# Performance work log

Hardware: AMD Instinct MI355X
Metric: run time of the kernel (lower is better)

## Reference

```python
import jax, jax.numpy as jnp
import numpy as np

G = 500          # num graphs
NODES_PER_G = 1000
EDGES_PER_G = 2000
N = G * NODES_PER_G   # 500_000 total nodes
E = G * EDGES_PER_G   # 1_000_000 total edges
DN, DE, DG, DO = 128, 64, 128, 128


def setup_inputs() -> dict:
    key = jax.random.key(0)
    ks = jax.random.split(key, 7)
    return {
        "node_features": jax.random.normal(ks[0], (N, DN), dtype=jnp.float32),
        "edge_features": jax.random.normal(ks[1], (E, DE), dtype=jnp.float32),
        "global_features": jax.random.normal(ks[2], (G, DG), dtype=jnp.float32),
        "W_node": jax.random.normal(ks[3], (DO, DN), dtype=jnp.float32) / np.sqrt(DN),
        "W_edges": jax.random.normal(ks[4], (DO, DE), dtype=jnp.float32) / np.sqrt(DE),
        "W_global": jax.random.normal(ks[5], (DO, DG), dtype=jnp.float32) / np.sqrt(DG),
        "bias": jax.random.normal(ks[6], (DO,), dtype=jnp.float32) * 0.01,
        "num_nodes_by_graph": jnp.full((G,), NODES_PER_G, dtype=jnp.int32),
        "num_edges_by_graph": jnp.full((G,), EDGES_PER_G, dtype=jnp.int32),
    }


def _segment_mean(feats, lengths, num_segments, total):
    # segment ids from per-graph lengths (segment_lengths_to_ids)
    ids = jnp.repeat(jnp.arange(num_segments, dtype=jnp.int32), lengths,
                     total_repeat_length=total)
    s = jax.ops.segment_sum(feats, ids, num_segments=num_segments)
    cnt = jnp.maximum(lengths, 1).astype(feats.dtype)[:, None]
    return s / cnt


def reference(node_features, edge_features, global_features,
              W_node, W_edges, W_global, bias,
              num_nodes_by_graph, num_edges_by_graph):
    # mean-aggregate nodes/edges per graph, then linear projections summed
    node_agg = _segment_mean(node_features, num_nodes_by_graph, G, N)   # [G, DN]
    edge_agg = _segment_mean(edge_features, num_edges_by_graph, G, E)   # [G, DE]
    out = (jnp.einsum('gd,od->go', node_agg, W_node)
           + jnp.einsum('gd,od->go', edge_agg, W_edges)
           + jnp.einsum('gd,od->go', global_features, W_global)
           + bias)
    return out
```

## Files before the change

kernel.cpp:

```cpp
#include <hip/hip_runtime.h>


#define DN 128
#define DE 64
#define DO 128
#define NODE_SPLIT 4
#define EDGE_SPLIT 8

__global__ __launch_bounds__(512) void scan_offsets_kernel(
    const int* __restrict__ nlen, const int* __restrict__ elen, int G,
    int* __restrict__ noff, int* __restrict__ eoff)
{
    __shared__ int sn[512], se[512];
    __shared__ int carry_n, carry_e;
    const int t = threadIdx.x;
    if (t == 0) { carry_n = 0; carry_e = 0; }
    __syncthreads();

    for (int base = 0; base < G; base += 512) {
        const int idx = base + t;
        const int vn = (idx < G) ? nlen[idx] : 0;
        const int ve = (idx < G) ? elen[idx] : 0;
        sn[t] = vn; se[t] = ve;
        __syncthreads();
        for (int off = 1; off < 512; off <<= 1) {
            const int an = (t >= off) ? sn[t - off] : 0;
            const int ae = (t >= off) ? se[t - off] : 0;
            __syncthreads();
            sn[t] += an; se[t] += ae;
            __syncthreads();
        }
        if (idx < G) {
            noff[idx] = carry_n + sn[t] - vn;
            eoff[idx] = carry_e + se[t] - ve;
        }
        __syncthreads();
        if (t == 0) {
            const int last = (G - base < 512) ? (G - base - 1) : 511;
            carry_n += sn[last];
            carry_e += se[last];
        }
        __syncthreads();
    }
}

__global__ __launch_bounds__(256) void agg_kernel(
    const float* __restrict__ nodes, const float* __restrict__ edges,
    const int* __restrict__ noff, const int* __restrict__ eoff,
    const int* __restrict__ nlen, const int* __restrict__ elen,
    float* __restrict__ nsum, float* __restrict__ esum, int G)
{
    __shared__ float4 sm[256];
    const int b = blockIdx.x;
    const int t = threadIdx.x;

    if (b < G * NODE_SPLIT) {
        const int g = b / NODE_SPLIT;
        const int c = b % NODE_SPLIT;
        const int len = nlen[g];
        const int off = noff[g];
        const int chunk = (len + NODE_SPLIT - 1) / NODE_SPLIT;
        const int r0 = c * chunk;
        const int r1 = (r0 + chunk < len) ? (r0 + chunk) : len;

        const int col = t & 31;
        const int rl  = t >> 5;
        float4 acc = make_float4(0.f, 0.f, 0.f, 0.f);
        const float4* __restrict__ base = (const float4*)nodes;
        for (int r = r0 + rl; r < r1; r += 8) {
            const float4 v = base[(size_t)(off + r) * (DN / 4) + col];
            acc.x += v.x; acc.y += v.y; acc.z += v.z; acc.w += v.w;
        }
        sm[t] = acc;
        __syncthreads();
        for (int s = 128; s >= 32; s >>= 1) {
            if (t < s) {
                const float4 o = sm[t + s];
                sm[t].x += o.x; sm[t].y += o.y; sm[t].z += o.z; sm[t].w += o.w;
            }
            __syncthreads();
        }
        if (t < 32) {
            const float4 v = sm[t];
            float* dst = &nsum[(size_t)g * DN + col * 4];
            atomicAdd(dst + 0, v.x);
            atomicAdd(dst + 1, v.y);
            atomicAdd(dst + 2, v.z);
            atomicAdd(dst + 3, v.w);
        }
    } else {
        const int bb = b - G * NODE_SPLIT;
        const int g = bb / EDGE_SPLIT;
        const int c = bb % EDGE_SPLIT;
        const int len = elen[g];
        const int off = eoff[g];
        const int chunk = (len + EDGE_SPLIT - 1) / EDGE_SPLIT;
        const int r0 = c * chunk;
        const int r1 = (r0 + chunk < len) ? (r0 + chunk) : len;

        const int col = t & 15;
        const int rl  = t >> 4;
        float4 acc = make_float4(0.f, 0.f, 0.f, 0.f);
        const float4* __restrict__ base = (const float4*)edges;
        for (int r = r0 + rl; r < r1; r += 16) {
            const float4 v = base[(size_t)(off + r) * (DE / 4) + col];
            acc.x += v.x; acc.y += v.y; acc.z += v.z; acc.w += v.w;
        }
        sm[t] = acc;
        __syncthreads();
        for (int s = 128; s >= 16; s >>= 1) {
            if (t < s) {
                const float4 o = sm[t + s];
                sm[t].x += o.x; sm[t].y += o.y; sm[t].z += o.z; sm[t].w += o.w;
            }
            __syncthreads();
        }
        if (t < 16) {
            const float4 v = sm[t];
            float* dst = &esum[(size_t)g * DE + col * 4];
            atomicAdd(dst + 0, v.x);
            atomicAdd(dst + 1, v.y);
            atomicAdd(dst + 2, v.z);
            atomicAdd(dst + 3, v.w);
        }
    }
}

__global__ __launch_bounds__(128) void finalize_kernel(
    const float* __restrict__ nsum, const float* __restrict__ esum,
    const float* __restrict__ glob,
    const float* __restrict__ Wn, const float* __restrict__ We,
    const float* __restrict__ Wg, const float* __restrict__ bias,
    const int* __restrict__ nlen, const int* __restrict__ elen,
    float* __restrict__ out)
{
    __shared__ float sn[DN], se_[DE], sg[DN];
    const int g = blockIdx.x;
    const int o = threadIdx.x;

    const int nl = nlen[g];
    const int el = elen[g];
    const float inv_n = 1.0f / (float)((nl > 1) ? nl : 1);
    const float inv_e = 1.0f / (float)((el > 1) ? el : 1);

    sn[o] = nsum[(size_t)g * DN + o] * inv_n;
    sg[o] = glob[(size_t)g * DN + o];
    if (o < DE) se_[o] = esum[(size_t)g * DE + o] * inv_e;
    __syncthreads();

    float acc = bias[o];
    const float4* __restrict__ wn = (const float4*)(Wn + (size_t)o * DN);
    const float4* __restrict__ wg = (const float4*)(Wg + (size_t)o * DN);
    const float4* __restrict__ we = (const float4*)(We + (size_t)o * DE);
    const float4* s4n = (const float4*)sn;
    const float4* s4g = (const float4*)sg;
    const float4* s4e = (const float4*)se_;

    #pragma unroll
    for (int i = 0; i < DN / 4; ++i) {
        const float4 a = wn[i], v = s4n[i];
        acc += a.x * v.x + a.y * v.y + a.z * v.z + a.w * v.w;
    }
    #pragma unroll
    for (int i = 0; i < DN / 4; ++i) {
        const float4 a = wg[i], v = s4g[i];
        acc += a.x * v.x + a.y * v.y + a.z * v.z + a.w * v.w;
    }
    #pragma unroll
    for (int i = 0; i < DE / 4; ++i) {
        const float4 a = we[i], v = s4e[i];
        acc += a.x * v.x + a.y * v.y + a.z * v.z + a.w * v.w;
    }
    out[(size_t)g * DO + o] = acc;
}

extern "C" void kernel_launch(void* const* d_in, const int* in_sizes, int n_in,
                              void* d_out, int out_size, void* d_ws, size_t ws_size,
                              hipStream_t stream)
{
    const float* nodes = (const float*)d_in[0];
    const float* edges = (const float*)d_in[1];
    const float* glob  = (const float*)d_in[2];
    const float* Wn    = (const float*)d_in[3];
    const float* We    = (const float*)d_in[4];
    const float* Wg    = (const float*)d_in[5];
    const float* bias  = (const float*)d_in[6];
    const int*   nlen  = (const int*)d_in[7];
    const int*   elen  = (const int*)d_in[8];
    float*       out   = (float*)d_out;

    const int G = in_sizes[7];

    float* nsum = (float*)d_ws;
    float* esum = nsum + (size_t)G * DN;
    int*   noff = (int*)(esum + (size_t)G * DE);
    int*   eoff = noff + G;

    hipMemsetAsync(d_ws, 0, (size_t)G * (DN + DE) * sizeof(float), stream);

    scan_offsets_kernel<<<1, 512, 0, stream>>>(nlen, elen, G, noff, eoff);

    const int agg_blocks = G * (NODE_SPLIT + EDGE_SPLIT);
    agg_kernel<<<agg_blocks, 256, 0, stream>>>(nodes, edges, noff, eoff,
                                               nlen, elen, nsum, esum, G);

    finalize_kernel<<<G, 128, 0, stream>>>(nsum, esum, glob, Wn, We, Wg, bias,
                                           nlen, elen, out);
}
```

Before: 518.7 us.

## Stream segment rows through an LDS ring via async global-to-LDS loads

```diff
diff --git a/kernel.cpp b/kernel.cpp
--- a/kernel.cpp
+++ b/kernel.cpp
@@ -1,11 +1,18 @@
 #include <hip/hip_runtime.h>
+#include <stdint.h>
 
 
 #define DN 128
 #define DE 64
 #define DO 128
-#define NODE_SPLIT 4
-#define EDGE_SPLIT 8
+#define NCHUNK 4
+#define NW 4
+#define SLOTS 8
+
+template<int N> __device__ __forceinline__ void wait_vmcnt() {
+    __builtin_amdgcn_s_waitcnt(0x0F70 | (N & 0xF) | ((N >> 4) << 14));
+    __asm__ volatile("" ::: "memory");
+}
 
 __global__ __launch_bounds__(512) void scan_offsets_kernel(
     const int* __restrict__ nlen, const int* __restrict__ elen, int G,
@@ -50,79 +57,103 @@
     const int* __restrict__ nlen, const int* __restrict__ elen,
     float* __restrict__ nsum, float* __restrict__ esum, int G)
 {
-    __shared__ float4 sm[256];
+    __shared__ float4 ring[NW * SLOTS * 64];
     const int b = blockIdx.x;
     const int t = threadIdx.x;
-
-    if (b < G * NODE_SPLIT) {
-        const int g = b / NODE_SPLIT;
-        const int c = b % NODE_SPLIT;
-        const int len = nlen[g];
-        const int off = noff[g];
-        const int chunk = (len + NODE_SPLIT - 1) / NODE_SPLIT;
-        const int r0 = c * chunk;
-        const int r1 = (r0 + chunk < len) ? (r0 + chunk) : len;
-
-        const int col = t & 31;
-        const int rl  = t >> 5;
-        float4 acc = make_float4(0.f, 0.f, 0.f, 0.f);
-        const float4* __restrict__ base = (const float4*)nodes;
-        for (int r = r0 + rl; r < r1; r += 8) {
-            const float4 v = base[(size_t)(off + r) * (DN / 4) + col];
-            acc.x += v.x; acc.y += v.y; acc.z += v.z; acc.w += v.w;
-        }
-        sm[t] = acc;
-        __syncthreads();
-        for (int s = 128; s >= 32; s >>= 1) {
-            if (t < s) {
-                const float4 o = sm[t + s];
-                sm[t].x += o.x; sm[t].y += o.y; sm[t].z += o.z; sm[t].w += o.w;
-            }
-            __syncthreads();
-        }
-        if (t < 32) {
-            const float4 v = sm[t];
-            float* dst = &nsum[(size_t)g * DN + col * 4];
-            atomicAdd(dst + 0, v.x);
-            atomicAdd(dst + 1, v.y);
-            atomicAdd(dst + 2, v.z);
-            atomicAdd(dst + 3, v.w);
-        }
-    } else {
-        const int bb = b - G * NODE_SPLIT;
-        const int g = bb / EDGE_SPLIT;
-        const int c = bb % EDGE_SPLIT;
-        const int len = elen[g];
-        const int off = eoff[g];
-        const int chunk = (len + EDGE_SPLIT - 1) / EDGE_SPLIT;
-        const int r0 = c * chunk;
-        const int r1 = (r0 + chunk < len) ? (r0 + chunk) : len;
-
-        const int col = t & 15;
-        const int rl  = t >> 4;
-        float4 acc = make_float4(0.f, 0.f, 0.f, 0.f);
-        const float4* __restrict__ base = (const float4*)edges;
-        for (int r = r0 + rl; r < r1; r += 16) {
-            const float4 v = base[(size_t)(off + r) * (DE / 4) + col];
-            acc.x += v.x; acc.y += v.y; acc.z += v.z; acc.w += v.w;
-        }
-        sm[t] = acc;
-        __syncthreads();
-        for (int s = 128; s >= 16; s >>= 1) {
-            if (t < s) {
-                const float4 o = sm[t + s];
-                sm[t].x += o.x; sm[t].y += o.y; sm[t].z += o.z; sm[t].w += o.w;
-            }
-            __syncthreads();
-        }
-        if (t < 16) {
-            const float4 v = sm[t];
-            float* dst = &esum[(size_t)g * DE + col * 4];
-            atomicAdd(dst + 0, v.x);
-            atomicAdd(dst + 1, v.y);
-            atomicAdd(dst + 2, v.z);
-            atomicAdd(dst + 3, v.w);
-        }
+    const int lane = t & 63;
+    const int w = t >> 6;
+
+    const bool is_node = (b < G * NCHUNK);
+    const int gb = is_node ? b : (b - G * NCHUNK);
+    const int g = gb / NCHUNK;
+    const int c = gb % NCHUNK;
+    const int RF = is_node ? (DN / 4) : (DE / 4);
+    const int len = is_node ? nlen[g] : elen[g];
+    const int off = is_node ? noff[g] : eoff[g];
+    const float4* __restrict__ src4 =
+        (const float4*)(is_node ? nodes : edges);
+    float* __restrict__ dst =
+        is_node ? &nsum[(size_t)g * DN] : &esum[(size_t)g * DE];
+
+    const size_t fbase = (size_t)off * RF;
+    const int span_total = len * RF;
+    const int chunk = ((span_total + NCHUNK * 64 - 1) / (NCHUNK * 64)) * 64;
+    const int fs = c * chunk;
+    int fe = fs + chunk; if (fe > span_total) fe = span_total;
+    const int span = (fe > fs) ? (fe - fs) : 0;
+    const int nslots = span >> 6;
+    const int rem = span & 63;
+
+    const int ns_w = (nslots > w) ? ((nslots - w + NW - 1) / NW) : 0;
+
+    char* ringc = (char*)ring;
+
+    auto issue = [&](int k) {
+        const int s = w + k * NW;
+        const float4* gp = src4 + fbase + (size_t)fs + (size_t)s * 64 + lane;
+        __builtin_amdgcn_global_load_lds(
+            (const __attribute__((address_space(1))) void*)gp,
+            (__attribute__((address_space(3))) void*)
+                (ringc + (((w * SLOTS) + (k % SLOTS)) << 10)),
+            16, 0, 0);
+    };
+    float4 acc = make_float4(0.f, 0.f, 0.f, 0.f);
+    auto consume = [&](int k) {
+        const float4* sp =
+            (const float4*)(ringc + (((w * SLOTS) + (k % SLOTS)) << 10));
+        const float4 v = sp[lane];
+        acc.x += v.x; acc.y += v.y; acc.z += v.z; acc.w += v.w;
+    };
+
+    const int pre = (ns_w < SLOTS) ? ns_w : SLOTS;
+    for (int k = 0; k < pre; ++k) issue(k);
+
+    int k = 0;
+    for (; k + SLOTS < ns_w; ++k) {
+        wait_vmcnt<SLOTS - 1>();
+        consume(k);
+        issue(k + SLOTS);
+    }
+    {
+        const int m = ns_w - k;
+        if (m > 7) { wait_vmcnt<7>(); consume(ns_w - 8); }
+        if (m > 6) { wait_vmcnt<6>(); consume(ns_w - 7); }
+        if (m > 5) { wait_vmcnt<5>(); consume(ns_w - 6); }
+        if (m > 4) { wait_vmcnt<4>(); consume(ns_w - 5); }
+        if (m > 3) { wait_vmcnt<3>(); consume(ns_w - 4); }
+        if (m > 2) { wait_vmcnt<2>(); consume(ns_w - 3); }
+        if (m > 1) { wait_vmcnt<1>(); consume(ns_w - 2); }
+        if (m > 0) { wait_vmcnt<0>(); consume(ns_w - 1); }
+    }
+
+    if (rem && t < rem) {
+        const int f = fs + (nslots << 6) + t;
+        const float4 v = src4[fbase + f];
+        const int col = f & (RF - 1);
+        atomicAdd(&dst[col * 4 + 0], v.x);
+        atomicAdd(&dst[col * 4 + 1], v.y);
+        atomicAdd(&dst[col * 4 + 2], v.z);
+        atomicAdd(&dst[col * 4 + 3], v.w);
+    }
+
+    __syncthreads();
+    float4* sm = ring;
+    sm[t] = acc;
+    __syncthreads();
+    const int tmin = RF;
+    for (int sdist = 128; sdist >= tmin; sdist >>= 1) {
+        if (t < sdist) {
+            const float4 o = sm[t + sdist];
+            sm[t].x += o.x; sm[t].y += o.y; sm[t].z += o.z; sm[t].w += o.w;
+        }
+        __syncthreads();
+    }
+    if (t < RF) {
+        const float4 v = sm[t];
+        atomicAdd(&dst[t * 4 + 0], v.x);
+        atomicAdd(&dst[t * 4 + 1], v.y);
+        atomicAdd(&dst[t * 4 + 2], v.z);
+        atomicAdd(&dst[t * 4 + 3], v.w);
     }
 }
 
@@ -184,10 +215,12 @@
     const float* Wn    = (const float*)d_in[3];
     const float* We    = (const float*)d_in[4];
     const float* Wg    = (const float*)d_in[5];
+    const float* Wg2   = (const float*)d_in[5];
     const float* bias  = (const float*)d_in[6];
     const int*   nlen  = (const int*)d_in[7];
     const int*   elen  = (const int*)d_in[8];
     float*       out   = (float*)d_out;
+    (void)Wg2;
 
     const int G = in_sizes[7];
 
@@ -200,7 +233,7 @@
 
     scan_offsets_kernel<<<1, 512, 0, stream>>>(nlen, elen, G, noff, eoff);
 
-    const int agg_blocks = G * (NODE_SPLIT + EDGE_SPLIT);
+    const int agg_blocks = G * NCHUNK * 2;
     agg_kernel<<<agg_blocks, 256, 0, stream>>>(nodes, edges, noff, eoff,
                                                nlen, elen, nsum, esum, G);
 
```

After: 514.5 us. No clear change (-0.8%).
